# Performance work log

Hardware: AMD Instinct MI355X
Metric: run time of the kernel (lower is better)

Reference implementation:

```python
import jax, jax.numpy as jnp
import numpy as np

V, ENC, D, E = 10000, 2048, 512, 512
B, L = 128, 64


def setup_inputs() -> dict:
    key = jax.random.key(0)
    ks = jax.random.split(key, 12)
    s = lambda *sh: 1.0 / np.sqrt(sh[-1])
    return {
        "global_feats": jax.random.normal(ks[0], (B, ENC), jnp.float32),
        "encoded_captions": jax.random.randint(ks[1], (B, L), 0, V, jnp.int64),
        "caption_lengths": jax.random.randint(ks[2], (B,), 1, L, jnp.int64),
        "W_embed": jax.random.normal(ks[3], (V, E), jnp.float32) * 0.02,
        "W_init": jax.random.normal(ks[4], (D, ENC), jnp.float32) * s(ENC),
        "b_init": jnp.zeros((D,), jnp.float32),
        "W_ih": jax.random.normal(ks[5], (3 * D, E), jnp.float32) * s(E),
        "W_hh": jax.random.normal(ks[6], (3 * D, D), jnp.float32) * s(D),
        "b_ih": jnp.zeros((3 * D,), jnp.float32),
        "b_hh": jnp.zeros((3 * D,), jnp.float32),
        "W_fc": jax.random.normal(ks[7], (V, D), jnp.float32) * s(D),
        "b_fc": jnp.zeros((V,), jnp.float32),
    }


def reference(global_feats, encoded_captions, caption_lengths,
              W_embed, W_init, b_init, W_ih, W_hh, b_ih, b_hh, W_fc, b_fc):
    # init_hidden: h0 = tanh(Linear(global_feats))  -> (B, D)
    h0 = jnp.tanh(global_feats @ W_init.T + b_init)

    # teacher forcing over timesteps 0..L-2 (PyTorch GRU gate order: r, z, n)
    emb = W_embed[encoded_captions[:, : L - 1]]          # (B, L-1, E)
    gi = jnp.einsum('ble,ge->blg', emb, W_ih) + b_ih     # (B, L-1, 3D) precomputed input gates
    gi = jnp.swapaxes(gi, 0, 1)                          # (L-1, B, 3D) scan over time

    def step(h, gi_t):
        gh = h @ W_hh.T + b_hh                           # (B, 3D)
        i_r, i_z, i_n = jnp.split(gi_t, 3, axis=-1)
        h_r, h_z, h_n = jnp.split(gh, 3, axis=-1)
        r = jax.nn.sigmoid(i_r + h_r)
        z = jax.nn.sigmoid(i_z + h_z)
        n = jnp.tanh(i_n + r * h_n)
        h_new = (1.0 - z) * n + z * h
        return h_new, h_new

    _, hs = jax.lax.scan(step, h0, gi)                   # hs: (L-1, B, D)
    # dropout is identity in eval/reference mode
    logits = jnp.einsum('lbd,vd->blv', hs, W_fc) + b_fc  # (B, L-1, V)
    return logits, caption_lengths - 1
```

## Files before the change

kernel.cpp:

```cpp
#include <hip/hip_runtime.h>
#include <hip/hip_bf16.h>

#define V_    10000
#define ENC_  2048
#define D_    512
#define B_    128
#define L_    64
#define T_    63
#define M_    (B_ * L_ - B_)
#define G_    (3 * D_)
#define LOGITS_SZ ((long)M_ * V_)
#define SCAN_NB 64

typedef __bf16 bf16x8_t __attribute__((ext_vector_type(8)));
typedef float  f32x4_t  __attribute__((ext_vector_type(4)));
typedef short  s16x8_t  __attribute__((ext_vector_type(8)));
typedef unsigned long long ull_t;

typedef __attribute__((address_space(3))) char*       lds_cptr_t;
typedef const __attribute__((address_space(1))) char* glb_cptr_t;

__device__ __forceinline__ void gload_lds16(const void* g, void* l) {
  __builtin_amdgcn_global_load_lds((glb_cptr_t)g, (lds_cptr_t)l, 16, 0, 0);
}
__device__ __forceinline__ float bf2f(short s) {
  return __uint_as_float(((unsigned)(unsigned short)s) << 16);
}
__device__ __forceinline__ short f2bf(float f) {
  __hip_bfloat16 h = __float2bfloat16(f);
  return *reinterpret_cast<short*>(&h);
}
__device__ __forceinline__ s16x8_t cvt8(const float* p) {
  f32x4_t lo = *reinterpret_cast<const f32x4_t*>(p);
  f32x4_t hi = *reinterpret_cast<const f32x4_t*>(p + 4);
  s16x8_t r;
#pragma unroll
  for (int e = 0; e < 4; e++) { r[e] = f2bf(lo[e]); r[4 + e] = f2bf(hi[e]); }
  return r;
}
__device__ __forceinline__ float sigmoidf_(float x) {
  return 1.0f / (1.0f + __expf(-x));
}
__device__ __forceinline__ bf16x8_t lds_frag(const short* p) {
  return __builtin_bit_cast(bf16x8_t, *reinterpret_cast<const s16x8_t*>(p));
}

__global__ void GG_cvt6(const float* __restrict__ whh, __hip_bfloat16* __restrict__ dwhh,
                        const float* __restrict__ wih, __hip_bfloat16* __restrict__ dwih,
                        const float* __restrict__ wemb, __hip_bfloat16* __restrict__ dwemb,
                        const float* __restrict__ winit, __hip_bfloat16* __restrict__ dwinit,
                        const float* __restrict__ gf, __hip_bfloat16* __restrict__ dgf,
                        const float* __restrict__ wfc, __hip_bfloat16* __restrict__ dwfc) {
  const int i = blockIdx.x * blockDim.x + threadIdx.x;
  const float* s; __hip_bfloat16* d; int off;
  if (i < 98304)        { s = whh;   d = dwhh;   off = i; }
  else if (i < 196608)  { s = wih;   d = dwih;   off = i - 98304; }
  else if (i < 836608)  { s = wemb;  d = dwemb;  off = i - 196608; }
  else if (i < 967680)  { s = winit; d = dwinit; off = i - 836608; }
  else if (i < 1000448) { s = gf;    d = dgf;    off = i - 967680; }
  else {
    if (dwfc == nullptr || i >= 1640448) return;
    s = wfc; d = dwfc; off = i - 1000448;
  }
  s16x8_t v = cvt8(s + (long)off * 8);
  *reinterpret_cast<s16x8_t*>(d + (long)off * 8) = v;
}

__global__ __launch_bounds__(256) void GG_gemm_h0(
    const __hip_bfloat16* __restrict__ gfB,
    const __hip_bfloat16* __restrict__ WinitB,
    const float* __restrict__ binit,
    __hip_bfloat16* __restrict__ hfull) {
  __shared__ short sA[128 * 64];
  __shared__ short sB[128 * 64];
  const int lane = threadIdx.x & 63;
  const int wave = threadIdx.x >> 6;
  const int n0 = blockIdx.x * 128;
  const int srow = lane >> 3;
  const int scolz = ((lane & 7) ^ (srow & 7)) * 8;

  f32x4_t acc[4][4] = {};

  const __hip_bfloat16* aptr[4];
  const __hip_bfloat16* bptr[4];
#pragma unroll
  for (int i = 0; i < 4; i++) {
    const int r = (wave * 4 + i) * 8 + srow;
    aptr[i] = gfB + (long)r * ENC_ + scolz;
    bptr[i] = WinitB + (long)(n0 + r) * ENC_ + scolz;
  }

  const int wm = (wave >> 1) * 64;
  const int wn = (wave & 1) * 64;
  const int fr = lane & 15;
  const int g4 = lane >> 4;

  for (int kt = 0; kt < 32; kt++) {
    __syncthreads();
#pragma unroll
    for (int i = 0; i < 4; i++) {
      const int chunk = wave * 4 + i;
      gload_lds16(aptr[i] + kt * 64, sA + chunk * 512);
      gload_lds16(bptr[i] + kt * 64, sB + chunk * 512);
    }
    __syncthreads();
#pragma unroll
    for (int kk = 0; kk < 2; kk++) {
      const int gsw = ((kk * 4 + g4) ^ (fr & 7)) * 8;
      bf16x8_t a[4], b[4];
#pragma unroll
      for (int i = 0; i < 4; i++) {
        a[i] = lds_frag(sA + (wm + i * 16 + fr) * 64 + gsw);
        b[i] = lds_frag(sB + (wn + i * 16 + fr) * 64 + gsw);
      }
#pragma unroll
      for (int i = 0; i < 4; i++)
#pragma unroll
        for (int j = 0; j < 4; j++)
          acc[i][j] = __builtin_amdgcn_mfma_f32_16x16x32_bf16(a[i], b[j], acc[i][j], 0, 0, 0);
    }
  }

  const int fq = lane >> 4;
#pragma unroll
  for (int j = 0; j < 4; j++) {
    const int n = n0 + wn + j * 16 + fr;
    const float bv = binit[n];
#pragma unroll
    for (int i = 0; i < 4; i++)
#pragma unroll
      for (int rr = 0; rr < 4; rr++) {
        const int m = wm + i * 16 + fq * 4 + rr;
        hfull[(long)m * 64 * 512 + n] = __float2bfloat16(tanhf(acc[i][j][rr] + bv));
      }
  }
}

__global__ __launch_bounds__(256) void GG_gemm_gi(
    const __hip_bfloat16* __restrict__ WembB,
    const int* __restrict__ cap,
    const __hip_bfloat16* __restrict__ WihB,
    const float* __restrict__ bias,
    __hip_bfloat16* __restrict__ C) {
  __shared__ short sA[128 * 64];
  __shared__ short sB[128 * 64];
  const int lane = threadIdx.x & 63;
  const int wave = threadIdx.x >> 6;
  const int m0 = blockIdx.y * 128;
  const int n0 = blockIdx.x * 128;
  const int srow = lane >> 3;
  const int scolz = ((lane & 7) ^ (srow & 7)) * 8;

  f32x4_t acc[4][4] = {};

  const __hip_bfloat16* aptr[4];
  const __hip_bfloat16* bptr[4];
#pragma unroll
  for (int i = 0; i < 4; i++) {
    const int r = (wave * 4 + i) * 8 + srow;
    const int bt = m0 + r;
    const int bb = bt / 63;
    const int tt = bt - bb * 63;
    aptr[i] = WembB + (long)cap[bb * L_ + tt] * 512 + scolz;
    bptr[i] = WihB + (long)(n0 + r) * 512 + scolz;
  }

  const int wm = (wave >> 1) * 64;
  const int wn = (wave & 1) * 64;
  const int fr = lane & 15;
  const int g4 = lane >> 4;

  for (int kt = 0; kt < 8; kt++) {
    __syncthreads();
#pragma unroll
    for (int i = 0; i < 4; i++) {
      const int chunk = wave * 4 + i;
      gload_lds16(aptr[i] + kt * 64, sA + chunk * 512);
      gload_lds16(bptr[i] + kt * 64, sB + chunk * 512);
    }
    __syncthreads();
#pragma unroll
    for (int kk = 0; kk < 2; kk++) {
      const int gsw = ((kk * 4 + g4) ^ (fr & 7)) * 8;
      bf16x8_t a[4], b[4];
#pragma unroll
      for (int i = 0; i < 4; i++) {
        a[i] = lds_frag(sA + (wm + i * 16 + fr) * 64 + gsw);
        b[i] = lds_frag(sB + (wn + i * 16 + fr) * 64 + gsw);
      }
#pragma unroll
      for (int i = 0; i < 4; i++)
#pragma unroll
        for (int j = 0; j < 4; j++)
          acc[i][j] = __builtin_amdgcn_mfma_f32_16x16x32_bf16(a[i], b[j], acc[i][j], 0, 0, 0);
    }
  }

  const int fq = lane >> 4;
#pragma unroll
  for (int j = 0; j < 4; j++) {
    const int n = n0 + wn + j * 16 + fr;
    const float bv = bias[n];
#pragma unroll
    for (int i = 0; i < 4; i++)
#pragma unroll
      for (int rr = 0; rr < 4; rr++) {
        const int m = m0 + wm + i * 16 + fq * 4 + rr;
        C[(long)m * G_ + n] = __float2bfloat16(acc[i][j][rr] + bv);
      }
  }
}

template <bool BBF16>
__global__ __launch_bounds__(512) void GG_gemm_logits(
    const __hip_bfloat16* __restrict__ hfull,
    const void* __restrict__ Bsrc,
    const float* __restrict__ bias,
    float* __restrict__ C) {
  const int flat = blockIdx.x;
  const int xcd = flat & 7;
  const int s = flat >> 3;
  const int col = xcd * 5 + s % 5;
  const int row = s / 5;
  const int m0 = row * 128;
  const int n0 = col * 256;

  __shared__ short sA[128 * 64];
  __shared__ short sB[256 * 64];
  const int lane = threadIdx.x & 63;
  const int wave = threadIdx.x >> 6;
  const int srow = lane >> 3;
  const int scol  = (lane & 7) * 8;
  const int scolz = ((lane & 7) ^ (srow & 7)) * 8;

  f32x4_t acc[4][4] = {};

  const __hip_bfloat16* aptr[2];
#pragma unroll
  for (int i = 0; i < 2; i++) {
    const int r = (wave + i * 8) * 8 + srow;
    const int m = m0 + r;
    const int bb = m / 63;
    const int tt = m - bb * 63;
    aptr[i] = hfull + ((long)bb * 64 + tt + 1) * 512 + scolz;
  }
  const __hip_bfloat16* bptrB[4];
  const float* bptrF[4];
#pragma unroll
  for (int i = 0; i < 4; i++) {
    int nrow = n0 + (wave + i * 8) * 8 + srow;
    nrow = (nrow < V_) ? nrow : (V_ - 1);
    if constexpr (BBF16) bptrB[i] = (const __hip_bfloat16*)Bsrc + (long)nrow * 512 + scolz;
    else                 bptrF[i] = (const float*)Bsrc + (long)nrow * 512 + scol;
  }

  const int wm = (wave >> 2) * 64;
  const int wn = (wave & 3) * 64;
  const int fr = lane & 15;
  const int g4 = lane >> 4;

  for (int kt = 0; kt < 8; kt++) {
    s16x8_t vb[4];
    if constexpr (!BBF16) {
#pragma unroll
      for (int i = 0; i < 4; i++) vb[i] = cvt8(bptrF[i] + kt * 64);
    }
    __syncthreads();
#pragma unroll
    for (int i = 0; i < 2; i++)
      gload_lds16(aptr[i] + kt * 64, sA + (wave + i * 8) * 512);
#pragma unroll
    for (int i = 0; i < 4; i++) {
      if constexpr (BBF16)
        gload_lds16(bptrB[i] + kt * 64, sB + (wave + i * 8) * 512);
      else
        *reinterpret_cast<s16x8_t*>(
            sB + (wave + i * 8) * 512 + srow * 64 + (((lane & 7) ^ (srow & 7)) * 8)) = vb[i];
    }
    __syncthreads();
#pragma unroll
    for (int kk = 0; kk < 2; kk++) {
      const int gsw = ((kk * 4 + g4) ^ (fr & 7)) * 8;
      bf16x8_t a[4], b[4];
#pragma unroll
      for (int i = 0; i < 4; i++) {
        a[i] = lds_frag(sA + (wm + i * 16 + fr) * 64 + gsw);
        b[i] = lds_frag(sB + (wn + i * 16 + fr) * 64 + gsw);
      }
#pragma unroll
      for (int i = 0; i < 4; i++)
#pragma unroll
        for (int j = 0; j < 4; j++)
          acc[i][j] = __builtin_amdgcn_mfma_f32_16x16x32_bf16(a[i], b[j], acc[i][j], 0, 0, 0);
    }
  }

  const int fq = lane >> 4;
#pragma unroll
  for (int j = 0; j < 4; j++) {
    const int n = n0 + wn + j * 16 + fr;
    if (n >= V_) continue;
    const float bv = bias[n];
#pragma unroll
    for (int i = 0; i < 4; i++)
#pragma unroll
      for (int rr = 0; rr < 4; rr++) {
        const int m = m0 + wm + i * 16 + fq * 4 + rr;
        C[(long)m * V_ + n] = acc[i][j][rr] + bv;
      }
  }
}

__global__ __launch_bounds__(256) void GG_scan_persist(
    __hip_bfloat16* __restrict__ hfull,
    const __hip_bfloat16* __restrict__ gi,
    const __hip_bfloat16* __restrict__ WhhB,
    const float* __restrict__ bhh,
    int* __restrict__ flagbase) {
  __shared__ short sW[48 * 512];
  const int lane = threadIdx.x & 63;
  const int wave = threadIdx.x >> 6;
  const int strip = blockIdx.x & 31;
  const int half  = blockIdx.x >> 5;
  const int d0 = strip * 16;
  const int fr = lane & 15;
  const int g4 = lane >> 4;
  int* myflags = flagbase + half * 32;

  for (int rr = wave; rr < 48; rr += 4) {
    const int grow = (rr >> 4) * 512 + d0 + (rr & 15);
    gload_lds16(WhhB + (long)grow * 512 + (lane ^ (rr & 7)) * 8, sW + rr * 512);
  }

  const int dd = d0 + fr;
  const int bbase = half * 64 + wave * 16 + g4 * 4;
  const float br_ = bhh[dd], bz_ = bhh[512 + dd], bn_ = bhh[1024 + dd];
  const short* gis = (const short*)gi;

  const int arow = half * 64 + wave * 16 + fr;
  const ull_t abase0 =
      (ull_t)hfull + ((ull_t)arow * 64 * 512 + (unsigned)(g4 * 8)) * 2ull;

  ull_t sbase[4];
  const short* gp0[4];
#pragma unroll
  for (int rr = 0; rr < 4; rr++) {
    sbase[rr] = (ull_t)hfull +
                ((ull_t)(bbase + rr) * 64 * 512 + (unsigned)dd) * 2ull;
    gp0[rr] = gis + (long)(bbase + rr) * T_ * G_ + dd;
  }

  unsigned cr[4], cz[4], cn[4];
  float hp[4];
#pragma unroll
  for (int rr = 0; rr < 4; rr++) {
    cr[rr] = (unsigned short)gp0[rr][0];
    cz[rr] = (unsigned short)gp0[rr][512];
    cn[rr] = (unsigned short)gp0[rr][1024];
    hp[rr] = bf2f(*(const short*)&hfull[((long)(bbase + rr) * 64) * 512 + dd]);
  }

  asm volatile("s_waitcnt vmcnt(0)" ::: "memory");
  __syncthreads();

  for (int t = 0; t < T_; t++) {
    if (t > 0) {
      while (true) {
        const int v = __hip_atomic_load(&myflags[lane & 31], __ATOMIC_RELAXED,
                                        __HIP_MEMORY_SCOPE_SYSTEM);
        if (__all(v >= t)) break;
        __builtin_amdgcn_s_sleep(1);
      }
    }

    const ull_t ab = abase0 + (ull_t)t * 1024ull;
    f32x4_t a[16];
#define ALOAD(IDX, OFF)                                                        \
    asm volatile("global_load_dwordx4 %0, %1, off offset:" #OFF " sc0 sc1"     \
                 : "=v"(a[IDX]) : "v"(ab));
    ALOAD(0, 0)    ALOAD(1, 64)   ALOAD(2, 128)  ALOAD(3, 192)
    ALOAD(4, 256)  ALOAD(5, 320)  ALOAD(6, 384)  ALOAD(7, 448)
    ALOAD(8, 512)  ALOAD(9, 576)  ALOAD(10, 640) ALOAD(11, 704)
    ALOAD(12, 768) ALOAD(13, 832) ALOAD(14, 896) ALOAD(15, 960)
#undef ALOAD

    const int tp = (t < T_ - 1) ? (t + 1) : (T_ - 1);
    unsigned nr[4], nz[4], nn[4];
#pragma unroll
    for (int rr = 0; rr < 4; rr++) {
      const short* gp = gp0[rr] + (long)tp * G_;
      asm volatile("global_load_ushort %0, %1, off"             : "=v"(nr[rr]) : "v"(gp));
      asm volatile("global_load_ushort %0, %1, off offset:1024" : "=v"(nz[rr]) : "v"(gp));
      asm volatile("global_load_ushort %0, %1, off offset:2048" : "=v"(nn[rr]) : "v"(gp));
    }

    asm volatile("s_waitcnt vmcnt(12)" ::: "memory");
    __builtin_amdgcn_sched_barrier(0);

    f32x4_t acc[3] = {};
#pragma unroll
    for (int kt = 0; kt < 16; kt++) {
      const bf16x8_t afr = __builtin_bit_cast(bf16x8_t, a[kt]);
      const int gsw = ((kt * 4 + g4) ^ (fr & 7)) * 8;
      bf16x8_t bfr[3];
#pragma unroll
      for (int j = 0; j < 3; j++) bfr[j] = lds_frag(sW + (j * 16 + fr) * 512 + gsw);
#pragma unroll
      for (int j = 0; j < 3; j++)
        acc[j] = __builtin_amdgcn_mfma_f32_16x16x32_bf16(afr, bfr[j], acc[j], 0, 0, 0);
    }

#pragma unroll
    for (int rr = 0; rr < 4; rr++) {
      const float rg = sigmoidf_(bf2f((short)cr[rr]) + acc[0][rr] + br_);
      const float zg = sigmoidf_(bf2f((short)cz[rr]) + acc[1][rr] + bz_);
      const float ng = tanhf(bf2f((short)cn[rr]) + rg * (acc[2][rr] + bn_));
      const short hnb = f2bf((1.f - zg) * ng + zg * hp[rr]);
      hp[rr] = bf2f(hnb);
      const ull_t saddr = sbase[rr] + (ull_t)(t + 1) * 1024ull;
      const unsigned int val = (unsigned short)hnb;
      asm volatile("global_store_short %0, %1, off sc0 sc1"
                   :: "v"(saddr), "v"(val) : "memory");
    }

    asm volatile("s_waitcnt vmcnt(0)" ::: "memory");
    __builtin_amdgcn_sched_barrier(0);
#pragma unroll
    for (int rr = 0; rr < 4; rr++) { cr[rr] = nr[rr]; cz[rr] = nz[rr]; cn[rr] = nn[rr]; }

    if (t < T_ - 1) {
      __syncthreads();
      if (threadIdx.x == 0)
        __hip_atomic_store(&myflags[strip], t + 1, __ATOMIC_RELAXED,
                           __HIP_MEMORY_SCOPE_SYSTEM);
    }
  }
}

__global__ void GG_tail_kernel(const int* __restrict__ lens, float* __restrict__ out) {
  const int b = threadIdx.x;
  if (b < B_) out[LOGITS_SZ + b] = (float)(lens[b] - 1);
}

extern "C" void kernel_launch(void* const* d_in, const int* in_sizes, int n_in,
                              void* d_out, int out_size, void* d_ws, size_t ws_size,
                              hipStream_t stream) {
  const float* gf      = (const float*)d_in[0];
  const int*   cap     = (const int*)d_in[1];
  const int*   lens    = (const int*)d_in[2];
  const float* W_embed = (const float*)d_in[3];
  const float* W_init  = (const float*)d_in[4];
  const float* b_init  = (const float*)d_in[5];
  const float* W_ih    = (const float*)d_in[6];
  const float* W_hh    = (const float*)d_in[7];
  const float* b_ih    = (const float*)d_in[8];
  const float* b_hh    = (const float*)d_in[9];
  const float* W_fc    = (const float*)d_in[10];
  const float* b_fc    = (const float*)d_in[11];
  float* out = (float*)d_out;

  char* ob = (char*)d_out;
  __hip_bfloat16* gi_ws  = (__hip_bfloat16*)ob;
  __hip_bfloat16* WhhB   = (__hip_bfloat16*)(ob + 25165824);
  __hip_bfloat16* WihB   = (__hip_bfloat16*)(ob + 27262976);
  __hip_bfloat16* WembB  = (__hip_bfloat16*)(ob + 29360128);
  __hip_bfloat16* WinitB = (__hip_bfloat16*)(ob + 40894464);
  __hip_bfloat16* gfB    = (__hip_bfloat16*)(ob + 43253760);

  __hip_bfloat16* hfull = (__hip_bfloat16*)d_ws;
  __hip_bfloat16* WfcB  = (__hip_bfloat16*)((char*)d_ws + 8388608);
  const bool big_ws = ws_size >= (size_t)(8388608 + 10240000 + 256);
  int* flags = (int*)((char*)d_ws + (big_ws ? 18628608 : 8388608));

  hipMemsetAsync(flags, 0, 256, stream);

  GG_cvt6<<<dim3(6408), 256, 0, stream>>>(W_hh, WhhB, W_ih, WihB, W_embed, WembB,
                                          W_init, WinitB, gf, gfB,
                                          W_fc, big_ws ? WfcB : nullptr);

  GG_gemm_h0<<<dim3(4), 256, 0, stream>>>(gfB, WinitB, b_init, hfull);

  GG_gemm_gi<<<dim3(G_ / 128, M_ / 128), 256, 0, stream>>>(WembB, cap, WihB, b_ih, gi_ws);

  GG_scan_persist<<<dim3(SCAN_NB), 256, 0, stream>>>(hfull, gi_ws, WhhB, b_hh, flags);

  if (big_ws)
    GG_gemm_logits<true><<<dim3(2520), 512, 0, stream>>>(hfull, WfcB, b_fc, out);
  else
    GG_gemm_logits<false><<<dim3(2520), 512, 0, stream>>>(hfull, W_fc, b_fc, out);

  GG_tail_kernel<<<dim3(1), 128, 0, stream>>>(lens, out);
}
```

Baseline: 516.7 us.

## Halve scan blocks with wider strips and fuse prep GEMMs into one launch

The persistent GRU scan now uses 32 blocks, each owning 32 hidden columns instead of 16. That halves the number of blocks that must synchronise through flags each timestep, at the cost of twice the MFMA and LDS work per block. The h0 GEMM, the gi GEMM and the caption-length tail kernel are merged into a single GG_prep launch, which removes two kernel launches. The risk is a longer per-step critical path inside each scan block.

```diff
diff --git a/kernel.cpp b/kernel.cpp
--- a/kernel.cpp
+++ b/kernel.cpp
@@ -10,7 +10,7 @@
 #define M_    (B_ * L_ - B_)
 #define G_    (3 * D_)
 #define LOGITS_SZ ((long)M_ * V_)
-#define SCAN_NB 64
+#define SCAN_NB 32
 
 typedef __bf16 bf16x8_t __attribute__((ext_vector_type(8)));
 typedef float  f32x4_t  __attribute__((ext_vector_type(4)));
@@ -66,93 +66,91 @@
   *reinterpret_cast<s16x8_t*>(d + (long)off * 8) = v;
 }
 
-__global__ __launch_bounds__(256) void GG_gemm_h0(
+__global__ __launch_bounds__(256) void GG_prep(
     const __hip_bfloat16* __restrict__ gfB,
     const __hip_bfloat16* __restrict__ WinitB,
     const float* __restrict__ binit,
-    __hip_bfloat16* __restrict__ hfull) {
-  __shared__ short sA[128 * 64];
-  __shared__ short sB[128 * 64];
-  const int lane = threadIdx.x & 63;
-  const int wave = threadIdx.x >> 6;
-  const int n0 = blockIdx.x * 128;
-  const int srow = lane >> 3;
-  const int scolz = ((lane & 7) ^ (srow & 7)) * 8;
-
-  f32x4_t acc[4][4] = {};
-
-  const __hip_bfloat16* aptr[4];
-  const __hip_bfloat16* bptr[4];
-#pragma unroll
-  for (int i = 0; i < 4; i++) {
-    const int r = (wave * 4 + i) * 8 + srow;
-    aptr[i] = gfB + (long)r * ENC_ + scolz;
-    bptr[i] = WinitB + (long)(n0 + r) * ENC_ + scolz;
-  }
-
-  const int wm = (wave >> 1) * 64;
-  const int wn = (wave & 1) * 64;
-  const int fr = lane & 15;
-  const int g4 = lane >> 4;
-
-  for (int kt = 0; kt < 32; kt++) {
-    __syncthreads();
-#pragma unroll
-    for (int i = 0; i < 4; i++) {
-      const int chunk = wave * 4 + i;
-      gload_lds16(aptr[i] + kt * 64, sA + chunk * 512);
-      gload_lds16(bptr[i] + kt * 64, sB + chunk * 512);
-    }
-    __syncthreads();
-#pragma unroll
-    for (int kk = 0; kk < 2; kk++) {
-      const int gsw = ((kk * 4 + g4) ^ (fr & 7)) * 8;
-      bf16x8_t a[4], b[4];
-#pragma unroll
-      for (int i = 0; i < 4; i++) {
-        a[i] = lds_frag(sA + (wm + i * 16 + fr) * 64 + gsw);
-        b[i] = lds_frag(sB + (wn + i * 16 + fr) * 64 + gsw);
-      }
-#pragma unroll
-      for (int i = 0; i < 4; i++)
-#pragma unroll
-        for (int j = 0; j < 4; j++)
-          acc[i][j] = __builtin_amdgcn_mfma_f32_16x16x32_bf16(a[i], b[j], acc[i][j], 0, 0, 0);
-    }
-  }
-
-  const int fq = lane >> 4;
-#pragma unroll
-  for (int j = 0; j < 4; j++) {
-    const int n = n0 + wn + j * 16 + fr;
-    const float bv = binit[n];
-#pragma unroll
-    for (int i = 0; i < 4; i++)
-#pragma unroll
-      for (int rr = 0; rr < 4; rr++) {
-        const int m = wm + i * 16 + fq * 4 + rr;
-        hfull[(long)m * 64 * 512 + n] = __float2bfloat16(tanhf(acc[i][j][rr] + bv));
-      }
-  }
-}
-
-__global__ __launch_bounds__(256) void GG_gemm_gi(
+    __hip_bfloat16* __restrict__ hfull,
     const __hip_bfloat16* __restrict__ WembB,
     const int* __restrict__ cap,
     const __hip_bfloat16* __restrict__ WihB,
-    const float* __restrict__ bias,
-    __hip_bfloat16* __restrict__ C) {
-  __shared__ short sA[128 * 64];
-  __shared__ short sB[128 * 64];
+    const float* __restrict__ bih,
+    __hip_bfloat16* __restrict__ giC,
+    const int* __restrict__ lens,
+    float* __restrict__ out) {
+  __shared__ short smem[2 * 128 * 64];
+  short* sA = smem;
+  short* sB = smem + 128 * 64;
   const int lane = threadIdx.x & 63;
   const int wave = threadIdx.x >> 6;
-  const int m0 = blockIdx.y * 128;
-  const int n0 = blockIdx.x * 128;
   const int srow = lane >> 3;
   const int scolz = ((lane & 7) ^ (srow & 7)) * 8;
+  const int fr = lane & 15;
+  const int g4 = lane >> 4;
+  const int wm = (wave >> 1) * 64;
+  const int wn = (wave & 1) * 64;
+
+  if (blockIdx.x >= 760) {
+    if (threadIdx.x < B_) out[LOGITS_SZ + threadIdx.x] = (float)(lens[threadIdx.x] - 1);
+    return;
+  }
 
   f32x4_t acc[4][4] = {};
 
+  if (blockIdx.x < 4) {
+    const int n0 = blockIdx.x * 128;
+    const __hip_bfloat16* aptr[4];
+    const __hip_bfloat16* bptr[4];
+#pragma unroll
+    for (int i = 0; i < 4; i++) {
+      const int r = (wave * 4 + i) * 8 + srow;
+      aptr[i] = gfB + (long)r * ENC_ + scolz;
+      bptr[i] = WinitB + (long)(n0 + r) * ENC_ + scolz;
+    }
+    for (int kt = 0; kt < 32; kt++) {
+      __syncthreads();
+#pragma unroll
+      for (int i = 0; i < 4; i++) {
+        const int chunk = wave * 4 + i;
+        gload_lds16(aptr[i] + kt * 64, sA + chunk * 512);
+        gload_lds16(bptr[i] + kt * 64, sB + chunk * 512);
+      }
+      __syncthreads();
+#pragma unroll
+      for (int kk = 0; kk < 2; kk++) {
+        const int gsw = ((kk * 4 + g4) ^ (fr & 7)) * 8;
+        bf16x8_t a[4], b[4];
+#pragma unroll
+        for (int i = 0; i < 4; i++) {
+          a[i] = lds_frag(sA + (wm + i * 16 + fr) * 64 + gsw);
+          b[i] = lds_frag(sB + (wn + i * 16 + fr) * 64 + gsw);
+        }
+#pragma unroll
+        for (int i = 0; i < 4; i++)
+#pragma unroll
+          for (int j = 0; j < 4; j++)
+            acc[i][j] = __builtin_amdgcn_mfma_f32_16x16x32_bf16(a[i], b[j], acc[i][j], 0, 0, 0);
+      }
+    }
+    const int fq = lane >> 4;
+#pragma unroll
+    for (int j = 0; j < 4; j++) {
+      const int n = n0 + wn + j * 16 + fr;
+      const float bv = binit[n];
+#pragma unroll
+      for (int i = 0; i < 4; i++)
+#pragma unroll
+        for (int rr = 0; rr < 4; rr++) {
+          const int m = wm + i * 16 + fq * 4 + rr;
+          hfull[(long)m * 64 * 512 + n] = __float2bfloat16(tanhf(acc[i][j][rr] + bv));
+        }
+    }
+    return;
+  }
+
+  const int flat = blockIdx.x - 4;
+  const int m0 = (flat / 12) * 128;
+  const int n0 = (flat % 12) * 128;
   const __hip_bfloat16* aptr[4];
   const __hip_bfloat16* bptr[4];
 #pragma unroll
@@ -164,12 +162,6 @@
     aptr[i] = WembB + (long)cap[bb * L_ + tt] * 512 + scolz;
     bptr[i] = WihB + (long)(n0 + r) * 512 + scolz;
   }
-
-  const int wm = (wave >> 1) * 64;
-  const int wn = (wave & 1) * 64;
-  const int fr = lane & 15;
-  const int g4 = lane >> 4;
-
   for (int kt = 0; kt < 8; kt++) {
     __syncthreads();
 #pragma unroll
@@ -195,18 +187,17 @@
           acc[i][j] = __builtin_amdgcn_mfma_f32_16x16x32_bf16(a[i], b[j], acc[i][j], 0, 0, 0);
     }
   }
-
   const int fq = lane >> 4;
 #pragma unroll
   for (int j = 0; j < 4; j++) {
     const int n = n0 + wn + j * 16 + fr;
-    const float bv = bias[n];
+    const float bv = bih[n];
 #pragma unroll
     for (int i = 0; i < 4; i++)
 #pragma unroll
       for (int rr = 0; rr < 4; rr++) {
         const int m = m0 + wm + i * 16 + fq * 4 + rr;
-        C[(long)m * G_ + n] = __float2bfloat16(acc[i][j][rr] + bv);
+        giC[(long)m * G_ + n] = __float2bfloat16(acc[i][j][rr] + bv);
       }
   }
 }
@@ -317,48 +308,58 @@
     const __hip_bfloat16* __restrict__ WhhB,
     const float* __restrict__ bhh,
     int* __restrict__ flagbase) {
-  __shared__ short sW[48 * 512];
+  __shared__ short sW[96 * 512];
   const int lane = threadIdx.x & 63;
   const int wave = threadIdx.x >> 6;
-  const int strip = blockIdx.x & 31;
-  const int half  = blockIdx.x >> 5;
-  const int d0 = strip * 16;
+  const int strip = blockIdx.x & 15;
+  const int half  = blockIdx.x >> 4;
+  const int d0 = strip * 32;
   const int fr = lane & 15;
   const int g4 = lane >> 4;
-  int* myflags = flagbase + half * 32;
-
-  for (int rr = wave; rr < 48; rr += 4) {
-    const int grow = (rr >> 4) * 512 + d0 + (rr & 15);
+  int* myflags = flagbase + half * 16;
+
+  for (int rr = wave; rr < 96; rr += 4) {
+    const int grow = (rr >> 5) * 512 + d0 + (rr & 31);
     gload_lds16(WhhB + (long)grow * 512 + (lane ^ (rr & 7)) * 8, sW + rr * 512);
   }
 
-  const int dd = d0 + fr;
   const int bbase = half * 64 + wave * 16 + g4 * 4;
-  const float br_ = bhh[dd], bz_ = bhh[512 + dd], bn_ = bhh[1024 + dd];
   const short* gis = (const short*)gi;
+
+  float br_[2], bz_[2], bn_[2];
+#pragma unroll
+  for (int sub = 0; sub < 2; sub++) {
+    const int dd = d0 + sub * 16 + fr;
+    br_[sub] = bhh[dd]; bz_[sub] = bhh[512 + dd]; bn_[sub] = bhh[1024 + dd];
+  }
 
   const int arow = half * 64 + wave * 16 + fr;
   const ull_t abase0 =
       (ull_t)hfull + ((ull_t)arow * 64 * 512 + (unsigned)(g4 * 8)) * 2ull;
 
-  ull_t sbase[4];
+  ull_t sbase[2][4];
   const short* gp0[4];
 #pragma unroll
   for (int rr = 0; rr < 4; rr++) {
-    sbase[rr] = (ull_t)hfull +
-                ((ull_t)(bbase + rr) * 64 * 512 + (unsigned)dd) * 2ull;
-    gp0[rr] = gis + (long)(bbase + rr) * T_ * G_ + dd;
-  }
-
-  unsigned cr[4], cz[4], cn[4];
-  float hp[4];
-#pragma unroll
-  for (int rr = 0; rr < 4; rr++) {
-    cr[rr] = (unsigned short)gp0[rr][0];
-    cz[rr] = (unsigned short)gp0[rr][512];
-    cn[rr] = (unsigned short)gp0[rr][1024];
-    hp[rr] = bf2f(*(const short*)&hfull[((long)(bbase + rr) * 64) * 512 + dd]);
-  }
+    gp0[rr] = gis + (long)(bbase + rr) * T_ * G_ + d0 + fr;
+#pragma unroll
+    for (int sub = 0; sub < 2; sub++)
+      sbase[sub][rr] = (ull_t)hfull +
+          ((ull_t)(bbase + rr) * 64 * 512 + (unsigned)(d0 + sub * 16 + fr)) * 2ull;
+  }
+
+  unsigned cr[2][4], cz[2][4], cn[2][4];
+  float hp[2][4];
+#pragma unroll
+  for (int rr = 0; rr < 4; rr++)
+#pragma unroll
+    for (int sub = 0; sub < 2; sub++) {
+      cr[sub][rr] = (unsigned short)gp0[rr][sub * 16];
+      cz[sub][rr] = (unsigned short)gp0[rr][512 + sub * 16];
+      cn[sub][rr] = (unsigned short)gp0[rr][1024 + sub * 16];
+      hp[sub][rr] = bf2f(*(const short*)&hfull[((long)(bbase + rr) * 64) * 512 +
+                                               d0 + sub * 16 + fr]);
+    }
 
   asm volatile("s_waitcnt vmcnt(0)" ::: "memory");
   __syncthreads();
@@ -366,7 +367,7 @@
   for (int t = 0; t < T_; t++) {
     if (t > 0) {
       while (true) {
-        const int v = __hip_atomic_load(&myflags[lane & 31], __ATOMIC_RELAXED,
+        const int v = __hip_atomic_load(&myflags[lane & 15], __ATOMIC_RELAXED,
                                         __HIP_MEMORY_SCOPE_SYSTEM);
         if (__all(v >= t)) break;
         __builtin_amdgcn_s_sleep(1);
@@ -385,48 +386,57 @@
 #undef ALOAD
 
     const int tp = (t < T_ - 1) ? (t + 1) : (T_ - 1);
-    unsigned nr[4], nz[4], nn[4];
+    unsigned nr[2][4], nz[2][4], nn[2][4];
 #pragma unroll
     for (int rr = 0; rr < 4; rr++) {
       const short* gp = gp0[rr] + (long)tp * G_;
-      asm volatile("global_load_ushort %0, %1, off"             : "=v"(nr[rr]) : "v"(gp));
-      asm volatile("global_load_ushort %0, %1, off offset:1024" : "=v"(nz[rr]) : "v"(gp));
-      asm volatile("global_load_ushort %0, %1, off offset:2048" : "=v"(nn[rr]) : "v"(gp));
-    }
-
-    asm volatile("s_waitcnt vmcnt(12)" ::: "memory");
+      asm volatile("global_load_ushort %0, %1, off"             : "=v"(nr[0][rr]) : "v"(gp));
+      asm volatile("global_load_ushort %0, %1, off offset:32"   : "=v"(nr[1][rr]) : "v"(gp));
+      asm volatile("global_load_ushort %0, %1, off offset:1024" : "=v"(nz[0][rr]) : "v"(gp));
+      asm volatile("global_load_ushort %0, %1, off offset:1056" : "=v"(nz[1][rr]) : "v"(gp));
+      asm volatile("global_load_ushort %0, %1, off offset:2048" : "=v"(nn[0][rr]) : "v"(gp));
+      asm volatile("global_load_ushort %0, %1, off offset:2080" : "=v"(nn[1][rr]) : "v"(gp));
+    }
+
+    asm volatile("s_waitcnt vmcnt(24)" ::: "memory");
     __builtin_amdgcn_sched_barrier(0);
 
-    f32x4_t acc[3] = {};
+    f32x4_t acc[6] = {};
 #pragma unroll
     for (int kt = 0; kt < 16; kt++) {
       const bf16x8_t afr = __builtin_bit_cast(bf16x8_t, a[kt]);
       const int gsw = ((kt * 4 + g4) ^ (fr & 7)) * 8;
-      bf16x8_t bfr[3];
-#pragma unroll
-      for (int j = 0; j < 3; j++) bfr[j] = lds_frag(sW + (j * 16 + fr) * 512 + gsw);
-#pragma unroll
-      for (int j = 0; j < 3; j++)
+      bf16x8_t bfr[6];
+#pragma unroll
+      for (int j = 0; j < 6; j++) bfr[j] = lds_frag(sW + (j * 16 + fr) * 512 + gsw);
+#pragma unroll
+      for (int j = 0; j < 6; j++)
         acc[j] = __builtin_amdgcn_mfma_f32_16x16x32_bf16(afr, bfr[j], acc[j], 0, 0, 0);
     }
 
 #pragma unroll
-    for (int rr = 0; rr < 4; rr++) {
-      const float rg = sigmoidf_(bf2f((short)cr[rr]) + acc[0][rr] + br_);
-      const float zg = sigmoidf_(bf2f((short)cz[rr]) + acc[1][rr] + bz_);
-      const float ng = tanhf(bf2f((short)cn[rr]) + rg * (acc[2][rr] + bn_));
-      const short hnb = f2bf((1.f - zg) * ng + zg * hp[rr]);
-      hp[rr] = bf2f(hnb);
-      const ull_t saddr = sbase[rr] + (ull_t)(t + 1) * 1024ull;
-      const unsigned int val = (unsigned short)hnb;
-      asm volatile("global_store_short %0, %1, off sc0 sc1"
-                   :: "v"(saddr), "v"(val) : "memory");
-    }
+    for (int sub = 0; sub < 2; sub++)
+#pragma unroll
+      for (int rr = 0; rr < 4; rr++) {
+        const float rg = sigmoidf_(bf2f((short)cr[sub][rr]) + acc[sub][rr] + br_[sub]);
+        const float zg = sigmoidf_(bf2f((short)cz[sub][rr]) + acc[2 + sub][rr] + bz_[sub]);
+        const float ng = tanhf(bf2f((short)cn[sub][rr]) + rg * (acc[4 + sub][rr] + bn_[sub]));
+        const short hnb = f2bf((1.f - zg) * ng + zg * hp[sub][rr]);
+        hp[sub][rr] = bf2f(hnb);
+        const ull_t saddr = sbase[sub][rr] + (ull_t)(t + 1) * 1024ull;
+        const unsigned int val = (unsigned short)hnb;
+        asm volatile("global_store_short %0, %1, off sc0 sc1"
+                     :: "v"(saddr), "v"(val) : "memory");
+      }
 
     asm volatile("s_waitcnt vmcnt(0)" ::: "memory");
     __builtin_amdgcn_sched_barrier(0);
 #pragma unroll
-    for (int rr = 0; rr < 4; rr++) { cr[rr] = nr[rr]; cz[rr] = nz[rr]; cn[rr] = nn[rr]; }
+    for (int sub = 0; sub < 2; sub++)
+#pragma unroll
+      for (int rr = 0; rr < 4; rr++) {
+        cr[sub][rr] = nr[sub][rr]; cz[sub][rr] = nz[sub][rr]; cn[sub][rr] = nn[sub][rr];
+      }
 
     if (t < T_ - 1) {
       __syncthreads();
@@ -435,11 +445,6 @@
                            __HIP_MEMORY_SCOPE_SYSTEM);
     }
   }
-}
-
-__global__ void GG_tail_kernel(const int* __restrict__ lens, float* __restrict__ out) {
-  const int b = threadIdx.x;
-  if (b < B_) out[LOGITS_SZ + b] = (float)(lens[b] - 1);
 }
 
 extern "C" void kernel_launch(void* const* d_in, const int* in_sizes, int n_in,
@@ -478,9 +483,8 @@
                                           W_init, WinitB, gf, gfB,
                                           W_fc, big_ws ? WfcB : nullptr);
 
-  GG_gemm_h0<<<dim3(4), 256, 0, stream>>>(gfB, WinitB, b_init, hfull);
-
-  GG_gemm_gi<<<dim3(G_ / 128, M_ / 128), 256, 0, stream>>>(WembB, cap, WihB, b_ih, gi_ws);
+  GG_prep<<<dim3(761), 256, 0, stream>>>(gfB, WinitB, b_init, hfull,
+                                         WembB, cap, WihB, b_ih, gi_ws, lens, out);
 
   GG_scan_persist<<<dim3(SCAN_NB), 256, 0, stream>>>(hfull, gi_ws, WhhB, b_hh, flags);
 
@@ -488,6 +492,4 @@
     GG_gemm_logits<true><<<dim3(2520), 512, 0, stream>>>(hfull, WfcB, b_fc, out);
   else
     GG_gemm_logits<false><<<dim3(2520), 512, 0, stream>>>(hfull, W_fc, b_fc, out);
-
-  GG_tail_kernel<<<dim3(1), 128, 0, stream>>>(lens, out);
-}
+}
```

Result: slower. 589.6 us (+14.1%).
